# Performance work log

Measured on AMD Instinct MI355X. Metric: run time of the kernel, lower is better.

The kernel has to match this reference:

```python
import jax, jax.numpy as jnp
import numpy as np

B, N, D = 8, 1024, 512
H = 8
DH = D // H
EPS_DIST = 1e-8
EPS_LN = 1e-5


def _layer_norm(x, gamma, beta):
    mu = jnp.mean(x, axis=-1, keepdims=True)
    var = jnp.mean((x - mu) ** 2, axis=-1, keepdims=True)
    return (x - mu) * jax.lax.rsqrt(var + EPS_LN) * gamma + beta


def setup_inputs() -> dict:
    key = jax.random.key(0)
    ks = jax.random.split(key, 6)
    scale = 1.0 / np.sqrt(D)
    inp = {
        "x": jax.random.normal(ks[0], (B, N, D), dtype=jnp.float32),
        "Wq": jax.random.normal(ks[1], (D, D), dtype=jnp.float32) * scale,
        "Wk": jax.random.normal(ks[2], (D, D), dtype=jnp.float32) * scale,
        "Wv": jax.random.normal(ks[3], (D, D), dtype=jnp.float32) * scale,
        "Wo": jax.random.normal(ks[4], (D, D), dtype=jnp.float32) * scale,
        "bq": jnp.zeros((D,), jnp.float32),
        "bk": jnp.zeros((D,), jnp.float32),
        "bv": jnp.zeros((D,), jnp.float32),
        "bo": jnp.zeros((D,), jnp.float32),
        "ln1_g": jnp.ones((D,), jnp.float32),
        "ln1_b": jnp.zeros((D,), jnp.float32),
        "ln2_g": jnp.ones((D,), jnp.float32),
        "ln2_b": jnp.zeros((D,), jnp.float32),
    }
    return inp


def reference(x, Wq, bq, Wk, bk, Wv, bv, Wo, bo, ln1_g, ln1_b, ln2_g, ln2_b):
    residual = x
    h = _layer_norm(x, ln1_g, ln1_b)  # pre-norm

    def heads(t):
        # [B,N,D] -> [B,H,N,DH]
        return t.reshape(B, N, H, DH).transpose(0, 2, 1, 3)

    q = heads(h @ Wq + bq)
    k = heads(h @ Wk + bk)
    v = heads(h @ Wv + bv)

    # Euclidean pairwise distance via ||q||^2 + ||k||^2 - 2 q.k expansion
    q_sq = jnp.sum(q * q, axis=-1)[..., :, None]      # [B,H,N,1]
    k_sq = jnp.sum(k * k, axis=-1)[..., None, :]      # [B,H,1,N]
    qk = jnp.einsum("bhnd,bhmd->bhnm", q, k)          # [B,H,N,N]
    d2 = jnp.maximum(q_sq + k_sq - 2.0 * qk, 0.0)
    dist = jnp.sqrt(d2 + EPS_DIST)

    # distance -> attention score: smaller distance = higher attention
    attn = jax.nn.softmax(-dist, axis=-1)             # [B,H,N,N]

    out = jnp.einsum("bhnm,bhmd->bhnd", attn, v)      # [B,H,N,DH]
    out = out.transpose(0, 2, 1, 3).reshape(B, N, D)
    out = out @ Wo + bo

    y = residual + out
    y = _layer_norm(y, ln2_g, ln2_b)
    return y
```

## Files before the change

### kernel.cpp

```cpp
#include <hip/hip_runtime.h>
#include <math.h>

typedef __attribute__((ext_vector_type(8))) short short8;
typedef __attribute__((ext_vector_type(4))) float f32x4;

constexpr int B  = 8;
constexpr int N  = 1024;
constexpr int D  = 512;
constexpr int H  = 8;
constexpr int DH = 64;
constexpr int M_ROWS = 8192;
constexpr float EPS_DIST = 1e-8f;
constexpr float EPS_LN   = 1e-5f;

__device__ inline unsigned short bfbits(float f) {
    union { float f; unsigned u; } v; v.f = f;
    unsigned r = v.u + 0x7fffu + ((v.u >> 16) & 1u);
    return (unsigned short)(r >> 16);
}
__device__ inline float bf2f(unsigned short s) {
    union { unsigned u; float f; } v; v.u = ((unsigned)s) << 16; return v.f;
}

__device__ inline void async_ld16(unsigned short* lds, const unsigned short* g) {
    __builtin_amdgcn_global_load_lds(
        (const __attribute__((address_space(1))) unsigned int*)(g),
        (__attribute__((address_space(3))) unsigned int*)(lds),
        16, 0, 0);
}

__device__ inline float block_sum256(float s, float* red) {
    for (int o = 32; o > 0; o >>= 1) s += __shfl_down(s, o, 64);
    int lane = threadIdx.x & 63, wid = threadIdx.x >> 6;
    if (lane == 0) red[wid] = s;
    __syncthreads();
    if (threadIdx.x == 0) red[4] = red[0] + red[1] + red[2] + red[3];
    __syncthreads();
    return red[4];
}

__global__ __launch_bounds__(256) void prep_kernel(const float* __restrict__ Wq,
                                                   const float* __restrict__ Wk,
                                                   const float* __restrict__ Wv,
                                                   const float* __restrict__ Wo,
                                                   unsigned short* __restrict__ WtAll,
                                                   const float* __restrict__ x,
                                                   const float* __restrict__ ln1_g,
                                                   const float* __restrict__ ln1_b,
                                                   unsigned short* __restrict__ h_bf) {
    __shared__ float red[8];
    const int bxg = blockIdx.x;
    if (bxg < 256) {
        int sub = bxg >> 6;
        const float* W = sub == 0 ? Wq : sub == 1 ? Wk : sub == 2 ? Wv : Wo;
        unsigned short* Wt = WtAll + (size_t)sub * 262144;
        int t = (bxg & 63) * 256 + threadIdx.x;
        int tn = t & 127, tk = t >> 7;
        int k = tk * 4, n = tn * 4;
        float4 r0 = *(const float4*)&W[(size_t)(k + 0) * 512 + n];
        float4 r1 = *(const float4*)&W[(size_t)(k + 1) * 512 + n];
        float4 r2 = *(const float4*)&W[(size_t)(k + 2) * 512 + n];
        float4 r3 = *(const float4*)&W[(size_t)(k + 3) * 512 + n];
        ushort4 c;
        c.x = bfbits(r0.x); c.y = bfbits(r1.x); c.z = bfbits(r2.x); c.w = bfbits(r3.x);
        *(ushort4*)&Wt[(size_t)(n + 0) * 512 + k] = c;
        c.x = bfbits(r0.y); c.y = bfbits(r1.y); c.z = bfbits(r2.y); c.w = bfbits(r3.y);
        *(ushort4*)&Wt[(size_t)(n + 1) * 512 + k] = c;
        c.x = bfbits(r0.z); c.y = bfbits(r1.z); c.z = bfbits(r2.z); c.w = bfbits(r3.z);
        *(ushort4*)&Wt[(size_t)(n + 2) * 512 + k] = c;
        c.x = bfbits(r0.w); c.y = bfbits(r1.w); c.z = bfbits(r2.w); c.w = bfbits(r3.w);
        *(ushort4*)&Wt[(size_t)(n + 3) * 512 + k] = c;
    } else {
        const int row = bxg - 256;
        const int t = threadIdx.x;
        const float* xr = x + (size_t)row * D;
        float v0 = xr[t], v1 = xr[t + 256];
        float mu = block_sum256(v0 + v1, red) * (1.0f / D);
        float d0 = v0 - mu, d1 = v1 - mu;
        float var = block_sum256(d0 * d0 + d1 * d1, red) * (1.0f / D);
        float rstd = rsqrtf(var + EPS_LN);
        h_bf[(size_t)row * D + t]       = bfbits(d0 * rstd * ln1_g[t] + ln1_b[t]);
        h_bf[(size_t)row * D + t + 256] = bfbits(d1 * rstd * ln1_g[t + 256] + ln1_b[t + 256]);
    }
}

__global__ __launch_bounds__(256) void ln2_kernel(const unsigned short* __restrict__ y0,
                                                  const float* __restrict__ res,
                                                  const float* __restrict__ gamma,
                                                  const float* __restrict__ beta,
                                                  float* __restrict__ out) {
    __shared__ float red[8];
    const int row = blockIdx.x;
    const int t = threadIdx.x;
    const unsigned short* xr = y0 + (size_t)row * D;
    const float* rr = res + (size_t)row * D;
    float v0 = bf2f(xr[t]) + rr[t];
    float v1 = bf2f(xr[t + 256]) + rr[t + 256];
    float mu = block_sum256(v0 + v1, red) * (1.0f / D);
    float d0 = v0 - mu, d1 = v1 - mu;
    float var = block_sum256(d0 * d0 + d1 * d1, red) * (1.0f / D);
    float rstd = rsqrtf(var + EPS_LN);
    out[(size_t)row * D + t]       = d0 * rstd * gamma[t] + beta[t];
    out[(size_t)row * D + t + 256] = d1 * rstd * gamma[t + 256] + beta[t + 256];
}

template <int MODE, int MT>
__global__ __launch_bounds__(256) void gemm128(const unsigned short* __restrict__ A,
                                               const unsigned short* __restrict__ Wt,
                                               const float* __restrict__ bias0,
                                               const float* __restrict__ bias1,
                                               const float* __restrict__ bias2,
                                               void* __restrict__ o0,
                                               unsigned short* __restrict__ Ko,
                                               unsigned short* __restrict__ Vo,
                                               float* __restrict__ sq0,
                                               float* __restrict__ sq1) {
    constexpr int RB = M_ROWS / MT;
    constexpr int NI = MT / 32;
    constexpr int ASZ = MT * 64, BSZ = 128 * 64;
    constexpr int SMSZ = (MODE == 1) ? ((ASZ + BSZ > 18432) ? ASZ + BSZ : 18432)
                                     : (ASZ + BSZ);
    __shared__ unsigned short smem[SMSZ];
    unsigned short* As = smem;
    unsigned short* Bs = smem + ASZ;

    const int id = blockIdx.x;
    const int by = id & (RB - 1), bx = id / RB;
    const int tid = threadIdx.x;
    const int lane = tid & 63, wv = tid >> 6;
    const int quad = lane >> 4, l15 = lane & 15;
    const int row0 = by * MT, col0 = bx * 128;
    const int wm = (wv & 1) * (MT / 2), wn = (wv >> 1) * 64;

    f32x4 acc[NI][4];
    #pragma unroll
    for (int i = 0; i < NI; ++i)
        #pragma unroll
        for (int j = 0; j < 4; ++j) acc[i][j] = (f32x4){0.f, 0.f, 0.f, 0.f};

    const unsigned short* Ag = A  + (size_t)row0 * 512;
    const unsigned short* Bg = Wt + (size_t)col0 * 512;

    for (int k0 = 0; k0 < 512; k0 += 64) {
        __syncthreads();
        #pragma unroll
        for (int c = 0; c < ASZ / 2048; ++c) {
            int fu = c * 2048 + tid * 8;
            int r = fu >> 6, ko = fu & 63;
            async_ld16(As + fu, Ag + (size_t)r * 512 + k0 + ko);
        }
        #pragma unroll
        for (int c = 0; c < BSZ / 2048; ++c) {
            int fu = c * 2048 + tid * 8;
            int r = fu >> 6, ko = fu & 63;
            async_ld16(Bs + fu, Bg + (size_t)r * 512 + k0 + ko);
        }
        __syncthreads();

        #pragma unroll
        for (int ks = 0; ks < 2; ++ks) {
            short8 af[NI], bf[4];
            #pragma unroll
            for (int i = 0; i < NI; ++i)
                af[i] = *(const short8*)&As[(wm + i * 16 + l15) * 64 + ks * 32 + quad * 8];
            #pragma unroll
            for (int j = 0; j < 4; ++j)
                bf[j] = *(const short8*)&Bs[(wn + j * 16 + l15) * 64 + ks * 32 + quad * 8];
            #pragma unroll
            for (int i = 0; i < NI; ++i)
                #pragma unroll
                for (int j = 0; j < 4; ++j)
                    acc[i][j] = __builtin_amdgcn_mfma_f32_16x16x32_bf16(af[i], bf[j], acc[i][j], 0, 0, 0);
        }
    }

    if (MODE == 0) {
        unsigned short* C = (unsigned short*)o0;
        #pragma unroll
        for (int i = 0; i < NI; ++i)
            #pragma unroll
            for (int j = 0; j < 4; ++j) {
                int col = col0 + wn + j * 16 + l15;
                float bv = bias0[col];
                #pragma unroll
                for (int r = 0; r < 4; ++r) {
                    int row = row0 + wm + i * 16 + quad * 4 + r;
                    C[(size_t)row * 512 + col] = bfbits(acc[i][j][r] + bv);
                }
            }
    } else {
        const int colg = col0 + wn;
        const int seg = colg >> 9;
        const int hh = (colg & 511) >> 6;
        const float* bias = seg == 0 ? bias0 : seg == 1 ? bias1 : bias2;

        if (seg < 2) {
            unsigned short* dst = seg == 0 ? (unsigned short*)o0 : Ko;
            float* sq = seg == 0 ? sq0 : sq1;
            #pragma unroll
            for (int i = 0; i < NI; ++i) {
                const int m0 = row0 + wm + i * 16 + quad * 4;
                float ss[4] = {0.f, 0.f, 0.f, 0.f};
                #pragma unroll
                for (int j = 0; j < 4; ++j) {
                    float bvj = bias[hh * 64 + j * 16 + l15];
                    #pragma unroll
                    for (int r = 0; r < 4; ++r) {
                        float v = acc[i][j][r] + bvj;
                        unsigned short ub = bfbits(v);
                        float vr = bf2f(ub);
                        ss[r] += vr * vr;
                        int m = m0 + r;
                        int b_ = m >> 10, n_ = m & 1023;
                        dst[((size_t)((b_ * 8 + hh) * 1024) + n_) * 64 + j * 16 + l15] = ub;
                    }
                }
                #pragma unroll
                for (int r = 0; r < 4; ++r) {
                    float s = ss[r];
                    s += __shfl_xor(s, 1, 64);
                    s += __shfl_xor(s, 2, 64);
                    s += __shfl_xor(s, 4, 64);
                    s += __shfl_xor(s, 8, 64);
                    if (l15 == 0) {
                        int m = m0 + r;
                        sq[(size_t)((m >> 10) * 8 + hh) * 1024 + (m & 1023)] = s;
                    }
                }
            }
        } else {
            __syncthreads();
            unsigned short* T = smem + wv * 4608;
            #pragma unroll
            for (int i = 0; i < NI; ++i)
                #pragma unroll
                for (int j = 0; j < 4; ++j) {
                    float bvj = bias[hh * 64 + j * 16 + l15];
                    ushort4 pk;
                    pk.x = bfbits(acc[i][j][0] + bvj);
                    pk.y = bfbits(acc[i][j][1] + bvj);
                    pk.z = bfbits(acc[i][j][2] + bvj);
                    pk.w = bfbits(acc[i][j][3] + bvj);
                    *(ushort4*)&T[(j * 16 + l15) * 72 + i * 16 + quad * 4] = pk;
                }
            const int b_ = (row0 + wm) >> 10;
            const int nbase = (row0 + wm) & 1023;
            unsigned short* Vg = Vo + ((size_t)((b_ * 8 + hh) * 64)) * 1024 + nbase;
            #pragma unroll
            for (int it = 0; it < 8; ++it) {
                int dl = it * 8 + (lane >> 3);
                int nl = (lane & 7) * 8;
                uint4 v = *(const uint4*)&T[dl * 72 + nl];
                *(uint4*)&Vg[(size_t)dl * 1024 + nl] = v;
            }
        }
    }
}

__global__ __launch_bounds__(512) void attn_kernel(const unsigned short* __restrict__ Q,
                                                   const unsigned short* __restrict__ K,
                                                   const unsigned short* __restrict__ Vt,
                                                   const float* __restrict__ qsq,
                                                   const float* __restrict__ ksq,
                                                   unsigned short* __restrict__ O) {
    __shared__ unsigned short Ks[2][64][72];
    __shared__ unsigned short Vs[2][64][72];
    __shared__ unsigned short Ps[8][16][72];
    __shared__ float ksq_s[2][64];

    const int id = blockIdx.x;
    const int bh = id & 63, qb = id >> 6;
    const int q0 = qb * 128;
    const int tid = threadIdx.x;
    const int lane = tid & 63, w = tid >> 6;
    const int quad = lane >> 4, l15 = lane & 15;
    const int b_ = bh >> 3, h_ = bh & 7;

    const unsigned short* Qb = Q  + (size_t)bh * N * DH;
    const unsigned short* Kb = K  + (size_t)bh * N * DH;
    const unsigned short* Vb = Vt + (size_t)bh * DH * N;

    short8 qf0, qf1;
    {
        const unsigned short* qp = Qb + (size_t)(q0 + w * 16 + l15) * 64 + quad * 8;
        qf0 = *(const short8*)qp;
        qf1 = *(const short8*)(qp + 32);
    }
    float qe[4];
    #pragma unroll
    for (int r = 0; r < 4; ++r)
        qe[r] = qsq[bh * N + q0 + w * 16 + quad * 4 + r] + EPS_DIST;

    f32x4 oacc[4];
    #pragma unroll
    for (int dt = 0; dt < 4; ++dt) oacc[dt] = (f32x4){0.f, 0.f, 0.f, 0.f};
    float dpart[4] = {};

    const int rr = tid >> 3, cc = (tid & 7) * 8;
    uint4 kreg, vreg;
    float ksreg = 0.f;

    kreg = *(const uint4*)(Kb + (size_t)rr * 64 + cc);
    vreg = *(const uint4*)(Vb + (size_t)rr * N + cc);
    if (tid < 64) ksreg = ksq[bh * N + tid];

    *(uint4*)&Ks[0][rr][cc] = kreg;
    *(uint4*)&Vs[0][rr][cc] = vreg;
    if (tid < 64) ksq_s[0][tid] = ksreg;
    __syncthreads();

    for (int kt = 0; kt < 16; ++kt) {
        const int cur = kt & 1;
        if (kt < 15) {
            kreg = *(const uint4*)(Kb + (size_t)((kt + 1) * 64 + rr) * 64 + cc);
            vreg = *(const uint4*)(Vb + (size_t)rr * N + (kt + 1) * 64 + cc);
            if (tid < 64) ksreg = ksq[bh * N + (kt + 1) * 64 + tid];
        }

        #pragma unroll
        for (int kb = 0; kb < 4; ++kb) {
            short8 kf0 = *(const short8*)&Ks[cur][kb * 16 + l15][quad * 8];
            short8 kf1 = *(const short8*)&Ks[cur][kb * 16 + l15][32 + quad * 8];
            float ks2 = ksq_s[cur][kb * 16 + l15];
            f32x4 sa = (f32x4){0.f, 0.f, 0.f, 0.f};
            sa = __builtin_amdgcn_mfma_f32_16x16x32_bf16(qf0, kf0, sa, 0, 0, 0);
            sa = __builtin_amdgcn_mfma_f32_16x16x32_bf16(qf1, kf1, sa, 0, 0, 0);
            #pragma unroll
            for (int r = 0; r < 4; ++r) {
                float d2 = fmaf(-2.0f, sa[r], qe[r] + ks2);
                d2 = fmaxf(d2, EPS_DIST);
                float p = __expf(-__builtin_amdgcn_sqrtf(d2));
                dpart[r] += p;
                union { float f; unsigned u; } pu; pu.f = p;
                Ps[w][quad * 4 + r][kb * 16 + l15] = (unsigned short)(pu.u >> 16);
            }
        }

        short8 vf[4][2];
        #pragma unroll
        for (int dt = 0; dt < 4; ++dt)
            #pragma unroll
            for (int kc = 0; kc < 2; ++kc)
                vf[dt][kc] = *(const short8*)&Vs[cur][dt * 16 + l15][kc * 32 + quad * 8];
        #pragma unroll
        for (int kc = 0; kc < 2; ++kc) {
            short8 pf = *(const short8*)&Ps[w][l15][kc * 32 + quad * 8];
            #pragma unroll
            for (int dt = 0; dt < 4; ++dt)
                oacc[dt] = __builtin_amdgcn_mfma_f32_16x16x32_bf16(pf, vf[dt][kc], oacc[dt], 0, 0, 0);
        }

        if (kt < 15) {
            *(uint4*)&Ks[cur ^ 1][rr][cc] = kreg;
            *(uint4*)&Vs[cur ^ 1][rr][cc] = vreg;
            if (tid < 64) ksq_s[cur ^ 1][tid] = ksreg;
        }
        __syncthreads();
    }

    float rinv[4];
    #pragma unroll
    for (int r = 0; r < 4; ++r) {
        float s = dpart[r];
        s += __shfl_xor(s, 1, 64);
        s += __shfl_xor(s, 2, 64);
        s += __shfl_xor(s, 4, 64);
        s += __shfl_xor(s, 8, 64);
        rinv[r] = 1.0f / s;
    }

    #pragma unroll
    for (int dt = 0; dt < 4; ++dt)
        #pragma unroll
        for (int r = 0; r < 4; ++r) {
            int n_ = q0 + w * 16 + quad * 4 + r;
            O[((size_t)(b_ * N + n_) * D) + h_ * DH + dt * 16 + l15] =
                bfbits(oacc[dt][r] * rinv[r]);
        }
}

extern "C" void kernel_launch(void* const* d_in, const int* in_sizes, int n_in,
                              void* d_out, int out_size, void* d_ws, size_t ws_size,
                              hipStream_t stream) {
    const float* x     = (const float*)d_in[0];
    const float* Wq    = (const float*)d_in[1];
    const float* Wk    = (const float*)d_in[2];
    const float* Wv    = (const float*)d_in[3];
    const float* Wo    = (const float*)d_in[4];
    const float* bq    = (const float*)d_in[5];
    const float* bk    = (const float*)d_in[6];
    const float* bv    = (const float*)d_in[7];
    const float* bo    = (const float*)d_in[8];
    const float* ln1_g = (const float*)d_in[9];
    const float* ln1_b = (const float*)d_in[10];
    const float* ln2_g = (const float*)d_in[11];
    const float* ln2_b = (const float*)d_in[12];
    float* out = (float*)d_out;

    unsigned short* WtAll = (unsigned short*)d_ws;
    unsigned short* h_bf  = WtAll + 4 * 262144;
    unsigned short* Qb    = h_bf + 4194304;
    unsigned short* Kb    = Qb + 4194304;
    unsigned short* Vtg   = Kb + 4194304;
    unsigned short* Ob    = Vtg + 4194304;
    unsigned short* Y0    = Ob + 4194304;
    float* qsq = (float*)(Y0 + 4194304);
    float* ksq = qsq + 65536;

    prep_kernel<<<256 + M_ROWS, 256, 0, stream>>>(Wq, Wk, Wv, Wo, WtAll,
                                                  x, ln1_g, ln1_b, h_bf);

    gemm128<1, 128><<<768, 256, 0, stream>>>(h_bf, WtAll, bq, bk, bv,
                                             Qb, Kb, Vtg, qsq, ksq);

    attn_kernel<<<512, 512, 0, stream>>>(Qb, Kb, Vtg, qsq, ksq, Ob);

    gemm128<0, 64><<<512, 256, 0, stream>>>(Ob, WtAll + 3 * 262144, bo,
                                            nullptr, nullptr, Y0,
                                            nullptr, nullptr, nullptr, nullptr);

    ln2_kernel<<<M_ROWS, 256, 0, stream>>>(Y0, x, ln2_g, ln2_b, out);
}
```

Before: 180.8 us.

## Give each attention wave two query tiles and use one wave per row for LayerNorms

The attention kernel drops from 8 waves to 4 per block, and each wave now handles 32 query rows (two 16-row MFMA tiles). Each K and V fragment loaded from LDS is therefore reused across twice as many MFMAs, and each thread loads two K/V chunks per stage. Both LayerNorm kernels now assign one wavefront per row, using float4 loads and xor-shuffle reductions instead of block-wide LDS reductions with barriers. The trade-off is more registers per wave in attention and half as many threads to hide latency.

```diff
diff --git a/kernel.cpp b/kernel.cpp
--- a/kernel.cpp
+++ b/kernel.cpp
@@ -27,16 +27,6 @@
         (const __attribute__((address_space(1))) unsigned int*)(g),
         (__attribute__((address_space(3))) unsigned int*)(lds),
         16, 0, 0);
-}
-
-__device__ inline float block_sum256(float s, float* red) {
-    for (int o = 32; o > 0; o >>= 1) s += __shfl_down(s, o, 64);
-    int lane = threadIdx.x & 63, wid = threadIdx.x >> 6;
-    if (lane == 0) red[wid] = s;
-    __syncthreads();
-    if (threadIdx.x == 0) red[4] = red[0] + red[1] + red[2] + red[3];
-    __syncthreads();
-    return red[4];
 }
 
 __global__ __launch_bounds__(256) void prep_kernel(const float* __restrict__ Wq,
@@ -48,7 +38,6 @@
                                                    const float* __restrict__ ln1_g,
                                                    const float* __restrict__ ln1_b,
                                                    unsigned short* __restrict__ h_bf) {
-    __shared__ float red[8];
     const int bxg = blockIdx.x;
     if (bxg < 256) {
         int sub = bxg >> 6;
@@ -71,16 +60,35 @@
         c.x = bfbits(r0.w); c.y = bfbits(r1.w); c.z = bfbits(r2.w); c.w = bfbits(r3.w);
         *(ushort4*)&Wt[(size_t)(n + 3) * 512 + k] = c;
     } else {
-        const int row = bxg - 256;
-        const int t = threadIdx.x;
-        const float* xr = x + (size_t)row * D;
-        float v0 = xr[t], v1 = xr[t + 256];
-        float mu = block_sum256(v0 + v1, red) * (1.0f / D);
-        float d0 = v0 - mu, d1 = v1 - mu;
-        float var = block_sum256(d0 * d0 + d1 * d1, red) * (1.0f / D);
-        float rstd = rsqrtf(var + EPS_LN);
-        h_bf[(size_t)row * D + t]       = bfbits(d0 * rstd * ln1_g[t] + ln1_b[t]);
-        h_bf[(size_t)row * D + t + 256] = bfbits(d1 * rstd * ln1_g[t + 256] + ln1_b[t + 256]);
+        const int w = threadIdx.x >> 6, lane = threadIdx.x & 63;
+        const int row = (bxg - 256) * 4 + w;
+        const float4* xr = (const float4*)(x + (size_t)row * D);
+        float4 a = xr[lane], b2 = xr[lane + 64];
+        float s = a.x + a.y + a.z + a.w + b2.x + b2.y + b2.z + b2.w;
+        #pragma unroll
+        for (int o = 1; o < 64; o <<= 1) s += __shfl_xor(s, o, 64);
+        const float mu = s * (1.0f / 512.0f);
+        float d0 = a.x - mu, d1 = a.y - mu, d2 = a.z - mu, d3 = a.w - mu;
+        float e0 = b2.x - mu, e1 = b2.y - mu, e2 = b2.z - mu, e3 = b2.w - mu;
+        float vs = d0*d0 + d1*d1 + d2*d2 + d3*d3 + e0*e0 + e1*e1 + e2*e2 + e3*e3;
+        #pragma unroll
+        for (int o = 1; o < 64; o <<= 1) vs += __shfl_xor(vs, o, 64);
+        const float rstd = rsqrtf(vs * (1.0f / 512.0f) + EPS_LN);
+        const float4* g4 = (const float4*)ln1_g;
+        const float4* b4 = (const float4*)ln1_b;
+        float4 ga = g4[lane], gb = g4[lane + 64];
+        float4 ba = b4[lane], bb = b4[lane + 64];
+        ushort4 u;
+        u.x = bfbits(d0 * rstd * ga.x + ba.x);
+        u.y = bfbits(d1 * rstd * ga.y + ba.y);
+        u.z = bfbits(d2 * rstd * ga.z + ba.z);
+        u.w = bfbits(d3 * rstd * ga.w + ba.w);
+        *(ushort4*)&h_bf[(size_t)row * 512 + lane * 4] = u;
+        u.x = bfbits(e0 * rstd * gb.x + bb.x);
+        u.y = bfbits(e1 * rstd * gb.y + bb.y);
+        u.z = bfbits(e2 * rstd * gb.z + bb.z);
+        u.w = bfbits(e3 * rstd * gb.w + bb.w);
+        *(ushort4*)&h_bf[(size_t)row * 512 + 256 + lane * 4] = u;
     }
 }
 
@@ -89,19 +97,38 @@
                                                   const float* __restrict__ gamma,
                                                   const float* __restrict__ beta,
                                                   float* __restrict__ out) {
-    __shared__ float red[8];
-    const int row = blockIdx.x;
-    const int t = threadIdx.x;
-    const unsigned short* xr = y0 + (size_t)row * D;
-    const float* rr = res + (size_t)row * D;
-    float v0 = bf2f(xr[t]) + rr[t];
-    float v1 = bf2f(xr[t + 256]) + rr[t + 256];
-    float mu = block_sum256(v0 + v1, red) * (1.0f / D);
-    float d0 = v0 - mu, d1 = v1 - mu;
-    float var = block_sum256(d0 * d0 + d1 * d1, red) * (1.0f / D);
-    float rstd = rsqrtf(var + EPS_LN);
-    out[(size_t)row * D + t]       = d0 * rstd * gamma[t] + beta[t];
-    out[(size_t)row * D + t + 256] = d1 * rstd * gamma[t + 256] + beta[t + 256];
+    const int w = threadIdx.x >> 6, lane = threadIdx.x & 63;
+    const int row = blockIdx.x * 4 + w;
+    const ushort4* y4 = (const ushort4*)(y0 + (size_t)row * D);
+    const float4*  r4 = (const float4*)(res + (size_t)row * D);
+    ushort4 ya = y4[lane], yb = y4[lane + 64];
+    float4  ra = r4[lane], rb = r4[lane + 64];
+    float v0 = bf2f(ya.x) + ra.x, v1 = bf2f(ya.y) + ra.y;
+    float v2 = bf2f(ya.z) + ra.z, v3 = bf2f(ya.w) + ra.w;
+    float v4 = bf2f(yb.x) + rb.x, v5 = bf2f(yb.y) + rb.y;
+    float v6 = bf2f(yb.z) + rb.z, v7 = bf2f(yb.w) + rb.w;
+    float s = v0 + v1 + v2 + v3 + v4 + v5 + v6 + v7;
+    #pragma unroll
+    for (int o = 1; o < 64; o <<= 1) s += __shfl_xor(s, o, 64);
+    const float mu = s * (1.0f / 512.0f);
+    v0 -= mu; v1 -= mu; v2 -= mu; v3 -= mu;
+    v4 -= mu; v5 -= mu; v6 -= mu; v7 -= mu;
+    float vs = v0*v0 + v1*v1 + v2*v2 + v3*v3 + v4*v4 + v5*v5 + v6*v6 + v7*v7;
+    #pragma unroll
+    for (int o = 1; o < 64; o <<= 1) vs += __shfl_xor(vs, o, 64);
+    const float rstd = rsqrtf(vs * (1.0f / 512.0f) + EPS_LN);
+    const float4* g4 = (const float4*)gamma;
+    const float4* b4 = (const float4*)beta;
+    float4 ga = g4[lane], gb = g4[lane + 64];
+    float4 ba = b4[lane], bb = b4[lane + 64];
+    float4 o1, o2;
+    o1.x = v0 * rstd * ga.x + ba.x; o1.y = v1 * rstd * ga.y + ba.y;
+    o1.z = v2 * rstd * ga.z + ba.z; o1.w = v3 * rstd * ga.w + ba.w;
+    o2.x = v4 * rstd * gb.x + bb.x; o2.y = v5 * rstd * gb.y + bb.y;
+    o2.z = v6 * rstd * gb.z + bb.z; o2.w = v7 * rstd * gb.w + bb.w;
+    float4* orow = (float4*)(out + (size_t)row * D);
+    orow[lane]      = o1;
+    orow[lane + 64] = o2;
 }
 
 template <int MODE, int MT>
@@ -257,7 +284,7 @@
     }
 }
 
-__global__ __launch_bounds__(512) void attn_kernel(const unsigned short* __restrict__ Q,
+__global__ __launch_bounds__(256) void attn_kernel(const unsigned short* __restrict__ Q,
                                                    const unsigned short* __restrict__ K,
                                                    const unsigned short* __restrict__ Vt,
                                                    const float* __restrict__ qsq,
@@ -265,7 +292,7 @@
                                                    unsigned short* __restrict__ O) {
     __shared__ unsigned short Ks[2][64][72];
     __shared__ unsigned short Vs[2][64][72];
-    __shared__ unsigned short Ps[8][16][72];
+    __shared__ unsigned short Ps[4][32][72];
     __shared__ float ksq_s[2][64];
 
     const int id = blockIdx.x;
@@ -280,40 +307,53 @@
     const unsigned short* Kb = K  + (size_t)bh * N * DH;
     const unsigned short* Vb = Vt + (size_t)bh * DH * N;
 
-    short8 qf0, qf1;
-    {
-        const unsigned short* qp = Qb + (size_t)(q0 + w * 16 + l15) * 64 + quad * 8;
-        qf0 = *(const short8*)qp;
-        qf1 = *(const short8*)(qp + 32);
+    short8 qf[2][2];
+    #pragma unroll
+    for (int qh = 0; qh < 2; ++qh) {
+        const unsigned short* qp = Qb + (size_t)(q0 + w * 32 + qh * 16 + l15) * 64 + quad * 8;
+        qf[qh][0] = *(const short8*)qp;
+        qf[qh][1] = *(const short8*)(qp + 32);
     }
-    float qe[4];
-    #pragma unroll
-    for (int r = 0; r < 4; ++r)
-        qe[r] = qsq[bh * N + q0 + w * 16 + quad * 4 + r] + EPS_DIST;
-
-    f32x4 oacc[4];
-    #pragma unroll
-    for (int dt = 0; dt < 4; ++dt) oacc[dt] = (f32x4){0.f, 0.f, 0.f, 0.f};
-    float dpart[4] = {};
-
-    const int rr = tid >> 3, cc = (tid & 7) * 8;
-    uint4 kreg, vreg;
+    float qe[2][4];
+    #pragma unroll
+    for (int qh = 0; qh < 2; ++qh)
+        #pragma unroll
+        for (int r = 0; r < 4; ++r)
+            qe[qh][r] = qsq[bh * N + q0 + w * 32 + qh * 16 + quad * 4 + r] + EPS_DIST;
+
+    f32x4 oacc[2][4];
+    #pragma unroll
+    for (int qh = 0; qh < 2; ++qh)
+        #pragma unroll
+        for (int dt = 0; dt < 4; ++dt) oacc[qh][dt] = (f32x4){0.f, 0.f, 0.f, 0.f};
+    float dpart[2][4] = {};
+
+    const int e0 = tid, e1 = tid + 256;
+    const int r0s = e0 >> 3, c0s = (e0 & 7) * 8;
+    const int r1s = e1 >> 3, c1s = (e1 & 7) * 8;
+    uint4 kreg0, kreg1, vreg0, vreg1;
     float ksreg = 0.f;
 
-    kreg = *(const uint4*)(Kb + (size_t)rr * 64 + cc);
-    vreg = *(const uint4*)(Vb + (size_t)rr * N + cc);
+    kreg0 = *(const uint4*)(Kb + (size_t)r0s * 64 + c0s);
+    kreg1 = *(const uint4*)(Kb + (size_t)r1s * 64 + c1s);
+    vreg0 = *(const uint4*)(Vb + (size_t)r0s * N + c0s);
+    vreg1 = *(const uint4*)(Vb + (size_t)r1s * N + c1s);
     if (tid < 64) ksreg = ksq[bh * N + tid];
 
-    *(uint4*)&Ks[0][rr][cc] = kreg;
-    *(uint4*)&Vs[0][rr][cc] = vreg;
+    *(uint4*)&Ks[0][r0s][c0s] = kreg0;
+    *(uint4*)&Ks[0][r1s][c1s] = kreg1;
+    *(uint4*)&Vs[0][r0s][c0s] = vreg0;
+    *(uint4*)&Vs[0][r1s][c1s] = vreg1;
     if (tid < 64) ksq_s[0][tid] = ksreg;
     __syncthreads();
 
     for (int kt = 0; kt < 16; ++kt) {
         const int cur = kt & 1;
         if (kt < 15) {
-            kreg = *(const uint4*)(Kb + (size_t)((kt + 1) * 64 + rr) * 64 + cc);
-            vreg = *(const uint4*)(Vb + (size_t)rr * N + (kt + 1) * 64 + cc);
+            kreg0 = *(const uint4*)(Kb + (size_t)((kt + 1) * 64 + r0s) * 64 + c0s);
+            kreg1 = *(const uint4*)(Kb + (size_t)((kt + 1) * 64 + r1s) * 64 + c1s);
+            vreg0 = *(const uint4*)(Vb + (size_t)r0s * N + (kt + 1) * 64 + c0s);
+            vreg1 = *(const uint4*)(Vb + (size_t)r1s * N + (kt + 1) * 64 + c1s);
             if (tid < 64) ksreg = ksq[bh * N + (kt + 1) * 64 + tid];
         }
 
@@ -322,17 +362,20 @@
             short8 kf0 = *(const short8*)&Ks[cur][kb * 16 + l15][quad * 8];
             short8 kf1 = *(const short8*)&Ks[cur][kb * 16 + l15][32 + quad * 8];
             float ks2 = ksq_s[cur][kb * 16 + l15];
-            f32x4 sa = (f32x4){0.f, 0.f, 0.f, 0.f};
-            sa = __builtin_amdgcn_mfma_f32_16x16x32_bf16(qf0, kf0, sa, 0, 0, 0);
-            sa = __builtin_amdgcn_mfma_f32_16x16x32_bf16(qf1, kf1, sa, 0, 0, 0);
-            #pragma unroll
-            for (int r = 0; r < 4; ++r) {
-                float d2 = fmaf(-2.0f, sa[r], qe[r] + ks2);
-                d2 = fmaxf(d2, EPS_DIST);
-                float p = __expf(-__builtin_amdgcn_sqrtf(d2));
-                dpart[r] += p;
-                union { float f; unsigned u; } pu; pu.f = p;
-                Ps[w][quad * 4 + r][kb * 16 + l15] = (unsigned short)(pu.u >> 16);
+            #pragma unroll
+            for (int qh = 0; qh < 2; ++qh) {
+                f32x4 sa = (f32x4){0.f, 0.f, 0.f, 0.f};
+                sa = __builtin_amdgcn_mfma_f32_16x16x32_bf16(qf[qh][0], kf0, sa, 0, 0, 0);
+                sa = __builtin_amdgcn_mfma_f32_16x16x32_bf16(qf[qh][1], kf1, sa, 0, 0, 0);
+                #pragma unroll
+                for (int r = 0; r < 4; ++r) {
+                    float d2 = fmaf(-2.0f, sa[r], qe[qh][r] + ks2);
+                    d2 = fmaxf(d2, EPS_DIST);
+                    float p = __expf(-__builtin_amdgcn_sqrtf(d2));
+                    dpart[qh][r] += p;
+                    union { float f; unsigned u; } pu; pu.f = p;
+                    Ps[w][qh * 16 + quad * 4 + r][kb * 16 + l15] = (unsigned short)(pu.u >> 16);
+                }
             }
         }
 
@@ -344,39 +387,48 @@
                 vf[dt][kc] = *(const short8*)&Vs[cur][dt * 16 + l15][kc * 32 + quad * 8];
         #pragma unroll
         for (int kc = 0; kc < 2; ++kc) {
-            short8 pf = *(const short8*)&Ps[w][l15][kc * 32 + quad * 8];
-            #pragma unroll
-            for (int dt = 0; dt < 4; ++dt)
-                oacc[dt] = __builtin_amdgcn_mfma_f32_16x16x32_bf16(pf, vf[dt][kc], oacc[dt], 0, 0, 0);
+            short8 pf0 = *(const short8*)&Ps[w][l15][kc * 32 + quad * 8];
+            short8 pf1 = *(const short8*)&Ps[w][16 + l15][kc * 32 + quad * 8];
+            #pragma unroll
+            for (int dt = 0; dt < 4; ++dt) {
+                oacc[0][dt] = __builtin_amdgcn_mfma_f32_16x16x32_bf16(pf0, vf[dt][kc], oacc[0][dt], 0, 0, 0);
+                oacc[1][dt] = __builtin_amdgcn_mfma_f32_16x16x32_bf16(pf1, vf[dt][kc], oacc[1][dt], 0, 0, 0);
+            }
         }
 
         if (kt < 15) {
-            *(uint4*)&Ks[cur ^ 1][rr][cc] = kreg;
-            *(uint4*)&Vs[cur ^ 1][rr][cc] = vreg;
+            *(uint4*)&Ks[cur ^ 1][r0s][c0s] = kreg0;
+            *(uint4*)&Ks[cur ^ 1][r1s][c1s] = kreg1;
+            *(uint4*)&Vs[cur ^ 1][r0s][c0s] = vreg0;
+            *(uint4*)&Vs[cur ^ 1][r1s][c1s] = vreg1;
             if (tid < 64) ksq_s[cur ^ 1][tid] = ksreg;
         }
         __syncthreads();
     }
 
-    float rinv[4];
-    #pragma unroll
-    for (int r = 0; r < 4; ++r) {
-        float s = dpart[r];
-        s += __shfl_xor(s, 1, 64);
-        s += __shfl_xor(s, 2, 64);
-        s += __shfl_xor(s, 4, 64);
-        s += __shfl_xor(s, 8, 64);
-        rinv[r] = 1.0f / s;
-    }
-
-    #pragma unroll
-    for (int dt = 0; dt < 4; ++dt)
+    float rinv[2][4];
+    #pragma unroll
+    for (int qh = 0; qh < 2; ++qh)
         #pragma unroll
         for (int r = 0; r < 4; ++r) {
-            int n_ = q0 + w * 16 + quad * 4 + r;
-            O[((size_t)(b_ * N + n_) * D) + h_ * DH + dt * 16 + l15] =
-                bfbits(oacc[dt][r] * rinv[r]);
-        }
+            float s = dpart[qh][r];
+            s += __shfl_xor(s, 1, 64);
+            s += __shfl_xor(s, 2, 64);
+            s += __shfl_xor(s, 4, 64);
+            s += __shfl_xor(s, 8, 64);
+            rinv[qh][r] = __builtin_amdgcn_rcpf(s);
+        }
+
+    #pragma unroll
+    for (int qh = 0; qh < 2; ++qh)
+        #pragma unroll
+        for (int dt = 0; dt < 4; ++dt)
+            #pragma unroll
+            for (int r = 0; r < 4; ++r) {
+                int n_ = q0 + w * 32 + qh * 16 + quad * 4 + r;
+                O[((size_t)(b_ * N + n_) * D) + h_ * DH + dt * 16 + l15] =
+                    bfbits(oacc[qh][dt][r] * rinv[qh][r]);
+            }
 }
 
 extern "C" void kernel_launch(void* const* d_in, const int* in_sizes, int n_in,
@@ -407,17 +459,17 @@
     float* qsq = (float*)(Y0 + 4194304);
     float* ksq = qsq + 65536;
 
-    prep_kernel<<<256 + M_ROWS, 256, 0, stream>>>(Wq, Wk, Wv, Wo, WtAll,
-                                                  x, ln1_g, ln1_b, h_bf);
+    prep_kernel<<<256 + M_ROWS / 4, 256, 0, stream>>>(Wq, Wk, Wv, Wo, WtAll,
+                                                      x, ln1_g, ln1_b, h_bf);
 
     gemm128<1, 128><<<768, 256, 0, stream>>>(h_bf, WtAll, bq, bk, bv,
                                              Qb, Kb, Vtg, qsq, ksq);
 
-    attn_kernel<<<512, 512, 0, stream>>>(Qb, Kb, Vtg, qsq, ksq, Ob);
+    attn_kernel<<<512, 256, 0, stream>>>(Qb, Kb, Vtg, qsq, ksq, Ob);
 
     gemm128<0, 64><<<512, 256, 0, stream>>>(Ob, WtAll + 3 * 262144, bo,
                                             nullptr, nullptr, Y0,
                                             nullptr, nullptr, nullptr, nullptr);
 
-    ln2_kernel<<<M_ROWS, 256, 0, stream>>>(Y0, x, ln2_g, ln2_b, out);
-}
+    ln2_kernel<<<M_ROWS / 4, 256, 0, stream>>>(Y0, x, ln2_g, ln2_b, out);
+}
```

New measurement: 180.1 us. No clear change (-0.4%).
